# Kernel optimization log

Hardware: AMD Instinct MI355X
Metric: run time of the kernel (lower is better)

The kernel has to match this reference:

```python
import jax, jax.numpy as jnp
import numpy as np

LN_EPS = 1e-5  # torch LayerNorm default


def setup_inputs() -> dict:
    key = jax.random.key(0)
    ks = jax.random.split(key, 6)
    N, E, D = 50000, 800000, 128
    x = jax.random.normal(ks[0], (N, D), dtype=jnp.float32)
    edge_index = jax.random.randint(ks[1], (2, E), 0, N, dtype=jnp.int64)
    # Linear params (torch default-ish init scale)
    W = jax.random.normal(ks[2], (D, D), dtype=jnp.float32) / np.sqrt(D)
    b = jax.random.normal(ks[3], (D,), dtype=jnp.float32) * 0.01
    # LayerNorm params
    gamma = jnp.ones((D,), dtype=jnp.float32)
    beta = jnp.zeros((D,), dtype=jnp.float32)
    return {"x": x, "edge_index": edge_index, "W": W, "b": b,
            "gamma": gamma, "beta": beta}


def reference(x, edge_index, W, b, gamma, beta):
    N = x.shape[0]
    # add_self_loops
    loops = jnp.arange(N, dtype=edge_index.dtype)
    row = jnp.concatenate([edge_index[0], loops])  # sources (x_j)
    col = jnp.concatenate([edge_index[1], loops])  # targets (aggregate here)

    h = x @ W.T + b  # [N, D]

    # symmetric normalization: deg computed on row, includes self loops (deg>=1)
    deg = jax.ops.segment_sum(jnp.ones(row.shape, dtype=h.dtype), row,
                              num_segments=N)
    dis = deg ** -0.5
    norm = dis[row] * dis[col]  # [E+N]

    # gather-scale-scatter message passing (aggr='add')
    msg = norm[:, None] * h[row]              # [E+N, D]
    agg = jax.ops.segment_sum(msg, col, num_segments=N)  # [N, D]

    out = jax.nn.relu(agg)
    # dropout: identity (eval mode)
    mu = jnp.mean(out, axis=-1, keepdims=True)
    var = jnp.var(out, axis=-1, keepdims=True)
    out = (out - mu) * jax.lax.rsqrt(var + LN_EPS) * gamma + beta
    return out + x  # residual (in_channels == out_channels, no proj)
```

## Files before the change

### kernel.cpp

```cpp
#include <hip/hip_runtime.h>


#define D 128
#define CHSH 15
#define CHUNK (1 << CHSH)
#define NWORD 12500

typedef short bf16x8 __attribute__((ext_vector_type(8)));
typedef float f32x4 __attribute__((ext_vector_type(4)));

__device__ __forceinline__ unsigned short f2bf(float f) {
    unsigned u = __float_as_uint(f);
    return (unsigned short)((u + 0x7fffu + ((u >> 16) & 1u)) >> 16);
}
__device__ __forceinline__ float bf2f_lo(unsigned v) { return __uint_as_float(v << 16); }
__device__ __forceinline__ float bf2f_hi(unsigned v) { return __uint_as_float(v & 0xffff0000u); }

__global__ void __launch_bounds__(1024)
k_gemm_hist(const float* __restrict__ x, const float* __restrict__ W,
            const float* __restrict__ bias, unsigned short* __restrict__ hb,
            int nrows,
            const int* __restrict__ ei, int E, int n,
            unsigned char* __restrict__ degc, unsigned char* __restrict__ cntc,
            unsigned char* __restrict__ aux, int K) {
    __shared__ unsigned sm[NWORD];
    int bid = blockIdx.x;
    if (bid < 2 * K) {
        unsigned* hist = sm;
        bool is_cnt = bid < K;
        int c = is_cnt ? bid : bid - K;
        const int* vs = is_cnt ? (ei + E) : ei;
        for (int i = threadIdx.x; i < NWORD; i += 1024) hist[i] = 0u;
        __syncthreads();
        int e0 = c << CHSH;
        int e1 = e0 + CHUNK; if (e1 > E) e1 = E;
        if (is_cnt) {
            for (int e = e0 + threadIdx.x; e < e1; e += 1024) {
                int v = vs[e];
                unsigned sh = (v & 3) * 8;
                unsigned old = atomicAdd(&hist[v >> 2], 1u << sh);
                aux[e] = (unsigned char)(old >> sh);
            }
        } else {
            for (int e = e0 + threadIdx.x; e < e1; e += 1024) {
                int v = vs[e];
                atomicAdd(&hist[v >> 2], 1u << ((v & 3) * 8));
            }
        }
        __syncthreads();
        unsigned* dst = (unsigned*)((is_cnt ? cntc : degc) + (size_t)c * n);
        for (int i = threadIdx.x; i < NWORD; i += 1024) dst[i] = hist[i];
    } else {
        unsigned short* wf = (unsigned short*)sm;
        for (int s = threadIdx.x; s < D * D; s += 1024) {
            int j  = s & 7;
            int ln = (s >> 3) & 63;
            int g  = s >> 9;
            int kt = g & 3, nt = g >> 2;
            int rw = nt * 16 + (ln & 15);
            int cl = kt * 32 + (ln >> 4) * 8 + j;
            wf[s] = f2bf(W[rw * D + cl]);
        }
        __syncthreads();

        int wid = threadIdx.x >> 6, lane = threadIdx.x & 63;
        int m0 = (bid - 2 * K) * 256 + wid * 16;
        if (m0 >= nrows) return;
        int lo16 = lane & 15, quad = lane >> 4;
        const float* arow = x + (size_t)(m0 + lo16) * D + quad * 8;
        bf16x8 a[4];
        #pragma unroll
        for (int kt = 0; kt < 4; kt++) {
            float4 p = *(const float4*)(arow + kt * 32);
            float4 q = *(const float4*)(arow + kt * 32 + 4);
            bf16x8 av;
            av[0] = (short)f2bf(p.x); av[1] = (short)f2bf(p.y);
            av[2] = (short)f2bf(p.z); av[3] = (short)f2bf(p.w);
            av[4] = (short)f2bf(q.x); av[5] = (short)f2bf(q.y);
            av[6] = (short)f2bf(q.z); av[7] = (short)f2bf(q.w);
            a[kt] = av;
        }
        const bf16x8* wfv = (const bf16x8*)sm;
        #pragma unroll
        for (int nt = 0; nt < 8; nt++) {
            int n0 = nt * 16;
            float bj = bias[n0 + lo16];
            f32x4 acc = {bj, bj, bj, bj};
            #pragma unroll
            for (int kt = 0; kt < 4; kt++) {
                bf16x8 b = wfv[(nt * 4 + kt) * 64 + lane];
                acc = __builtin_amdgcn_mfma_f32_16x16x32_bf16(a[kt], b, acc, 0, 0, 0);
            }
            #pragma unroll
            for (int r = 0; r < 4; r++) {
                int gr = m0 + quad * 4 + r;
                hb[(size_t)gr * D + n0 + lo16] = f2bf(acc[r]);
            }
        }
    }
}

__global__ void k_partial(const unsigned char* __restrict__ degc,
                          const unsigned char* __restrict__ cntc,
                          float* __restrict__ dis, unsigned* __restrict__ cnt,
                          unsigned* __restrict__ partial, int n, int K) {
    __shared__ unsigned s[256];
    int t = threadIdx.x;
    int i = blockIdx.x * 256 + t;
    unsigned tot = 0;
    if (i < n) {
        unsigned d = 0;
        for (int c = 0; c < K; c++)
            d += __builtin_nontemporal_load(degc + (size_t)c * n + i);
        dis[i] = rsqrtf((float)d + 1.0f);
        for (int c = 0; c < K; c++) tot += cntc[(size_t)c * n + i];
        cnt[i] = tot;
    }
    s[t] = tot;
    __syncthreads();
    #pragma unroll
    for (int d = 128; d > 0; d >>= 1) {
        if (t < d) s[t] += s[t + d];
        __syncthreads();
    }
    if (t == 0) partial[blockIdx.x] = s[0];
}

__global__ void k_rowptrc(const unsigned* __restrict__ cnt, const unsigned char* __restrict__ cntc,
                          const unsigned* __restrict__ partial, int n, int E,
                          int* __restrict__ rowptr, unsigned char* __restrict__ pre8,
                          int K, int nb) {
    __shared__ unsigned ps[256];
    __shared__ unsigned base_sh;
    int t = threadIdx.x;
    unsigned pv = (t < nb) ? partial[t] : 0u;
    ps[t] = pv;
    __syncthreads();
    #pragma unroll
    for (int d = 1; d < 256; d <<= 1) {
        unsigned u = (t >= d) ? ps[t - d] : 0u;
        __syncthreads();
        ps[t] += u;
        __syncthreads();
    }
    if (t == blockIdx.x) base_sh = ps[t] - pv;
    __syncthreads();
    unsigned bbase = base_sh;
    int i = blockIdx.x * 256 + t;
    unsigned v = (i < n) ? cnt[i] : 0u;
    ps[t] = v;
    __syncthreads();
    #pragma unroll
    for (int d = 1; d < 256; d <<= 1) {
        unsigned u = (t >= d) ? ps[t - d] : 0u;
        __syncthreads();
        ps[t] += u;
        __syncthreads();
    }
    if (i < n) {
        int base = (int)(bbase + ps[t] - v);
        rowptr[i] = base;
        unsigned run = 0;
        for (int c = 0; c < K; c++) {
            pre8[(size_t)c * n + i] = (unsigned char)run;
            run += cntc[(size_t)c * n + i];
        }
    }
    if (blockIdx.x == 0 && t == 0) rowptr[n] = E;
}

__global__ void k_fill(const int* __restrict__ ei, int E, int n,
                       const int* __restrict__ rowptr, const unsigned char* __restrict__ pre8,
                       const unsigned char* __restrict__ aux,
                       unsigned short* __restrict__ srcs) {
    int e = blockIdx.x * 256 + threadIdx.x;
    if (e < E) {
        int r = __builtin_nontemporal_load(ei + e);
        int v = __builtin_nontemporal_load(ei + E + e);
        int c = e >> CHSH;
        int rank = __builtin_nontemporal_load(aux + e);
        int base = rowptr[v] + (int)pre8[(size_t)c * n + v];
        srcs[base + rank] = (unsigned short)r;
    }
}

__global__ void k_agg(const float* __restrict__ x, const unsigned short* __restrict__ hb,
                      const float* __restrict__ dis,
                      const int* __restrict__ rowptr, const unsigned short* __restrict__ srcs,
                      const float* __restrict__ gamma, const float* __restrict__ beta,
                      float* __restrict__ out, int n) {
    int wid = threadIdx.x >> 6, lane = threadIdx.x & 63;
    int row = blockIdx.x * 4 + wid;
    if (row >= n) return;
    int q = lane >> 4, t = lane & 15;
    float dc = dis[row];
    float acc[8];
    #pragma unroll
    for (int i = 0; i < 8; i++) acc[i] = 0.0f;
    if (q == 0) {
        uint4 u = ((const uint4*)(hb + (size_t)row * D))[t];
        float sn = dc * dc;
        acc[0] = sn * bf2f_lo(u.x); acc[1] = sn * bf2f_hi(u.x);
        acc[2] = sn * bf2f_lo(u.y); acc[3] = sn * bf2f_hi(u.y);
        acc[4] = sn * bf2f_lo(u.z); acc[5] = sn * bf2f_hi(u.z);
        acc[6] = sn * bf2f_lo(u.w); acc[7] = sn * bf2f_hi(u.w);
    }
    int s0 = rowptr[row];
    int len = rowptr[row + 1] - s0;
    for (int base = 0; base < len; base += 64) {
        int idx = base + lane;
        int sv = (idx < len) ? (int)__builtin_nontemporal_load(srcs + s0 + idx) : 0;
        float dv = (idx < len) ? dis[sv] : 0.0f;
        int m = len - base; if (m > 64) m = 64;
        int kmax = (m + 3) >> 2;
        int gcount = (kmax + 3) >> 2;
        for (int gg = 0; gg < gcount; gg++) {
            int jb = q + (gg << 4);
            int r0 = __shfl(sv, jb, 64);
            int r1 = __shfl(sv, jb + 4, 64);
            int r2 = __shfl(sv, jb + 8, 64);
            int r3 = __shfl(sv, jb + 12, 64);
            float w0 = dc * __shfl(dv, jb, 64);
            float w1 = dc * __shfl(dv, jb + 4, 64);
            float w2 = dc * __shfl(dv, jb + 8, 64);
            float w3 = dc * __shfl(dv, jb + 12, 64);
            uint4 u0 = ((const uint4*)(hb + ((size_t)r0 << 7)))[t];
            uint4 u1 = ((const uint4*)(hb + ((size_t)r1 << 7)))[t];
            uint4 u2 = ((const uint4*)(hb + ((size_t)r2 << 7)))[t];
            uint4 u3 = ((const uint4*)(hb + ((size_t)r3 << 7)))[t];
            acc[0] += w0 * bf2f_lo(u0.x); acc[1] += w0 * bf2f_hi(u0.x);
            acc[2] += w0 * bf2f_lo(u0.y); acc[3] += w0 * bf2f_hi(u0.y);
            acc[4] += w0 * bf2f_lo(u0.z); acc[5] += w0 * bf2f_hi(u0.z);
            acc[6] += w0 * bf2f_lo(u0.w); acc[7] += w0 * bf2f_hi(u0.w);
            acc[0] += w1 * bf2f_lo(u1.x); acc[1] += w1 * bf2f_hi(u1.x);
            acc[2] += w1 * bf2f_lo(u1.y); acc[3] += w1 * bf2f_hi(u1.y);
            acc[4] += w1 * bf2f_lo(u1.z); acc[5] += w1 * bf2f_hi(u1.z);
            acc[6] += w1 * bf2f_lo(u1.w); acc[7] += w1 * bf2f_hi(u1.w);
            acc[0] += w2 * bf2f_lo(u2.x); acc[1] += w2 * bf2f_hi(u2.x);
            acc[2] += w2 * bf2f_lo(u2.y); acc[3] += w2 * bf2f_hi(u2.y);
            acc[4] += w2 * bf2f_lo(u2.z); acc[5] += w2 * bf2f_hi(u2.z);
            acc[6] += w2 * bf2f_lo(u2.w); acc[7] += w2 * bf2f_hi(u2.w);
            acc[0] += w3 * bf2f_lo(u3.x); acc[1] += w3 * bf2f_hi(u3.x);
            acc[2] += w3 * bf2f_lo(u3.y); acc[3] += w3 * bf2f_hi(u3.y);
            acc[4] += w3 * bf2f_lo(u3.z); acc[5] += w3 * bf2f_hi(u3.z);
            acc[6] += w3 * bf2f_lo(u3.w); acc[7] += w3 * bf2f_hi(u3.w);
        }
    }
    #pragma unroll
    for (int i = 0; i < 8; i++) {
        acc[i] += __shfl_xor(acc[i], 16, 64);
        acc[i] += __shfl_xor(acc[i], 32, 64);
        acc[i] = acc[i] > 0.0f ? acc[i] : 0.0f;
    }
    float s1r = 0.0f, s2r = 0.0f;
    #pragma unroll
    for (int i = 0; i < 8; i++) { s1r += acc[i]; s2r += acc[i] * acc[i]; }
    #pragma unroll
    for (int mm = 8; mm >= 1; mm >>= 1) {
        s1r += __shfl_xor(s1r, mm, 64);
        s2r += __shfl_xor(s2r, mm, 64);
    }
    float mean = s1r * (1.0f / 128.0f);
    float var  = s2r * (1.0f / 128.0f) - mean * mean;
    float rstd = rsqrtf(var + 1e-5f);
    if (q == 0) {
        const f32x4* gr = (const f32x4*)gamma;
        const f32x4* br = (const f32x4*)beta;
        const f32x4* xr = (const f32x4*)(x + (size_t)row * D);
        f32x4* orow = (f32x4*)(out + (size_t)row * D);
        #pragma unroll
        for (int hf = 0; hf < 2; hf++) {
            f32x4 g = gr[2 * t + hf], b = br[2 * t + hf];
            f32x4 xx = __builtin_nontemporal_load(xr + 2 * t + hf);
            f32x4 o;
            o[0] = (acc[4 * hf + 0] - mean) * rstd * g[0] + b[0] + xx[0];
            o[1] = (acc[4 * hf + 1] - mean) * rstd * g[1] + b[1] + xx[1];
            o[2] = (acc[4 * hf + 2] - mean) * rstd * g[2] + b[2] + xx[2];
            o[3] = (acc[4 * hf + 3] - mean) * rstd * g[3] + b[3] + xx[3];
            __builtin_nontemporal_store(o, orow + 2 * t + hf);
        }
    }
}

extern "C" void kernel_launch(void* const* d_in, const int* in_sizes, int n_in,
                              void* d_out, int out_size, void* d_ws, size_t ws_size,
                              hipStream_t stream) {
    const float* x     = (const float*)d_in[0];
    const int*   ei    = (const int*)d_in[1];
    const float* W     = (const float*)d_in[2];
    const float* bias  = (const float*)d_in[3];
    const float* gamma = (const float*)d_in[4];
    const float* beta  = (const float*)d_in[5];
    int N = in_sizes[0] / D;
    int E = in_sizes[1] / 2;
    int nb  = (N + 255) / 256;
    int nbE = (E + 255) / 256;
    int K   = (E + CHUNK - 1) >> CHSH;
    int gemm_blocks = (N + 255) / 256;

    char* ws = (char*)d_ws;
    size_t off = 0;
    unsigned short* hb  = (unsigned short*)(ws + off); off += (size_t)N * D * 2;
    unsigned char* degc = (unsigned char*)(ws + off);  off += (size_t)K * N;
    unsigned char* cntc = (unsigned char*)(ws + off);  off += (size_t)K * N;
    float*    dis       = (float*)(ws + off);          off += (size_t)N * 4;
    unsigned* cnt       = (unsigned*)(ws + off);       off += (size_t)N * 4;
    int*      rowptr    = (int*)(ws + off);            off += (size_t)(N + 1) * 4;
    unsigned char* pre8 = (unsigned char*)(ws + off);  off += (size_t)K * N;
    unsigned* partial   = (unsigned*)(ws + off);       off += 256 * 4;
    unsigned char* aux  = (unsigned char*)(ws + off);  off += (size_t)E;
    off = (off + 1) & ~(size_t)1;
    unsigned short* srcs = (unsigned short*)(ws + off); off += (size_t)E * 2;
    float*    out       = (float*)d_out;

    k_gemm_hist<<<2 * K + gemm_blocks, 1024, 0, stream>>>(x, W, bias, hb, N,
                                                          ei, E, N, degc, cntc, aux, K);
    k_partial<<<nb, 256, 0, stream>>>(degc, cntc, dis, cnt, partial, N, K);
    k_rowptrc<<<nb, 256, 0, stream>>>(cnt, cntc, partial, N, E, rowptr, pre8, K, nb);
    k_fill<<<nbE, 256, 0, stream>>>(ei, E, N, rowptr, pre8, aux, srcs);
    k_agg<<<(N + 3) / 4, 256, 0, stream>>>(x, hb, dis, rowptr, srcs, gamma, beta, out, N);
}
```

Baseline: 177.0 us.

## Fuse post-GEMM stages into one cooperative kernel with grid syncs

Merges the degree/partial-sum, row-pointer scan, CSR fill and aggregation+LayerNorm kernels into a single persistent cooperative kernel that uses grid.sync between phases. The goal is to remove three kernel launch boundaries and their launch/drain overhead. In exchange, the grid is limited to the number of co-resident blocks, so the aggregation phase loops over rows with fewer blocks, and each grid barrier has its own cost. If the cooperative launch fails, it falls back to the old separate kernels.

```diff
diff --git a/kernel.cpp b/kernel.cpp
--- a/kernel.cpp
+++ b/kernel.cpp
@@ -1,4 +1,7 @@
 #include <hip/hip_runtime.h>
+#include <hip/hip_cooperative_groups.h>
+
+namespace cg = cooperative_groups;
 
 
 #define D 128
@@ -95,6 +98,189 @@
             for (int r = 0; r < 4; r++) {
                 int gr = m0 + quad * 4 + r;
                 hb[(size_t)gr * D + n0 + lo16] = f2bf(acc[r]);
+            }
+        }
+    }
+}
+
+__global__ void __launch_bounds__(256, 8)
+k_coop(const float* __restrict__ x, const unsigned short* __restrict__ hb,
+       const unsigned char* __restrict__ degc, const unsigned char* __restrict__ cntc,
+       const unsigned char* __restrict__ aux, const int* __restrict__ ei,
+       float* __restrict__ dis, unsigned* __restrict__ cnt,
+       int* __restrict__ rowptr, unsigned char* __restrict__ pre8,
+       unsigned* __restrict__ partial, unsigned short* __restrict__ srcs,
+       const float* __restrict__ gamma, const float* __restrict__ beta,
+       float* __restrict__ out, int n, int E, int K, int nb) {
+    cg::grid_group grid = cg::this_grid();
+    int bid = blockIdx.x, t = threadIdx.x;
+    int NB = gridDim.x;
+    __shared__ unsigned ps[256];
+    __shared__ unsigned base_sh;
+
+    for (int b = bid; b < nb; b += NB) {
+        int i = b * 256 + t;
+        unsigned tot = 0;
+        if (i < n) {
+            unsigned d = 0;
+            for (int c = 0; c < K; c++)
+                d += __builtin_nontemporal_load(degc + (size_t)c * n + i);
+            dis[i] = rsqrtf((float)d + 1.0f);
+            for (int c = 0; c < K; c++) tot += cntc[(size_t)c * n + i];
+            cnt[i] = tot;
+        }
+        ps[t] = tot;
+        __syncthreads();
+        #pragma unroll
+        for (int d = 128; d > 0; d >>= 1) {
+            if (t < d) ps[t] += ps[t + d];
+            __syncthreads();
+        }
+        if (t == 0) partial[b] = ps[0];
+        __syncthreads();
+    }
+    grid.sync();
+
+    for (int b = bid; b < nb; b += NB) {
+        unsigned pv = (t < nb) ? partial[t] : 0u;
+        ps[t] = pv;
+        __syncthreads();
+        #pragma unroll
+        for (int d = 1; d < 256; d <<= 1) {
+            unsigned u = (t >= d) ? ps[t - d] : 0u;
+            __syncthreads();
+            ps[t] += u;
+            __syncthreads();
+        }
+        if (t == b) base_sh = ps[t] - pv;
+        __syncthreads();
+        unsigned bbase = base_sh;
+        int i = b * 256 + t;
+        unsigned v = (i < n) ? cnt[i] : 0u;
+        ps[t] = v;
+        __syncthreads();
+        #pragma unroll
+        for (int d = 1; d < 256; d <<= 1) {
+            unsigned u = (t >= d) ? ps[t - d] : 0u;
+            __syncthreads();
+            ps[t] += u;
+            __syncthreads();
+        }
+        if (i < n) {
+            int base = (int)(bbase + ps[t] - v);
+            rowptr[i] = base;
+            unsigned run = 0;
+            for (int c = 0; c < K; c++) {
+                pre8[(size_t)c * n + i] = (unsigned char)run;
+                run += cntc[(size_t)c * n + i];
+            }
+        }
+        if (b == 0 && t == 0) rowptr[n] = E;
+        __syncthreads();
+    }
+    grid.sync();
+
+    for (int e = bid * 256 + t; e < E; e += NB * 256) {
+        int r = __builtin_nontemporal_load(ei + e);
+        int v = __builtin_nontemporal_load(ei + E + e);
+        int c = e >> CHSH;
+        int rank = __builtin_nontemporal_load(aux + e);
+        int base = rowptr[v] + (int)pre8[(size_t)c * n + v];
+        srcs[base + rank] = (unsigned short)r;
+    }
+    grid.sync();
+
+    int wid = t >> 6, lane = t & 63;
+    int q = lane >> 4, tt = lane & 15;
+    int nrg = (n + 3) >> 2;
+    for (int rg = bid; rg < nrg; rg += NB) {
+        int row = rg * 4 + wid;
+        if (row >= n) continue;
+        float dc = dis[row];
+        float acc[8];
+        #pragma unroll
+        for (int i = 0; i < 8; i++) acc[i] = 0.0f;
+        if (q == 0) {
+            uint4 u = ((const uint4*)(hb + (size_t)row * D))[tt];
+            float sn = dc * dc;
+            acc[0] = sn * bf2f_lo(u.x); acc[1] = sn * bf2f_hi(u.x);
+            acc[2] = sn * bf2f_lo(u.y); acc[3] = sn * bf2f_hi(u.y);
+            acc[4] = sn * bf2f_lo(u.z); acc[5] = sn * bf2f_hi(u.z);
+            acc[6] = sn * bf2f_lo(u.w); acc[7] = sn * bf2f_hi(u.w);
+        }
+        int s0 = rowptr[row];
+        int len = rowptr[row + 1] - s0;
+        for (int base = 0; base < len; base += 64) {
+            int idx = base + lane;
+            int sv = (idx < len) ? (int)__builtin_nontemporal_load(srcs + s0 + idx) : 0;
+            float dv = (idx < len) ? dis[sv] : 0.0f;
+            int m = len - base; if (m > 64) m = 64;
+            int kmax = (m + 3) >> 2;
+            int gcount = (kmax + 3) >> 2;
+            for (int gg = 0; gg < gcount; gg++) {
+                int jb = q + (gg << 4);
+                int r0 = __shfl(sv, jb, 64);
+                int r1 = __shfl(sv, jb + 4, 64);
+                int r2 = __shfl(sv, jb + 8, 64);
+                int r3 = __shfl(sv, jb + 12, 64);
+                float w0 = dc * __shfl(dv, jb, 64);
+                float w1 = dc * __shfl(dv, jb + 4, 64);
+                float w2 = dc * __shfl(dv, jb + 8, 64);
+                float w3 = dc * __shfl(dv, jb + 12, 64);
+                uint4 u0 = ((const uint4*)(hb + ((size_t)r0 << 7)))[tt];
+                uint4 u1 = ((const uint4*)(hb + ((size_t)r1 << 7)))[tt];
+                uint4 u2 = ((const uint4*)(hb + ((size_t)r2 << 7)))[tt];
+                uint4 u3 = ((const uint4*)(hb + ((size_t)r3 << 7)))[tt];
+                acc[0] += w0 * bf2f_lo(u0.x); acc[1] += w0 * bf2f_hi(u0.x);
+                acc[2] += w0 * bf2f_lo(u0.y); acc[3] += w0 * bf2f_hi(u0.y);
+                acc[4] += w0 * bf2f_lo(u0.z); acc[5] += w0 * bf2f_hi(u0.z);
+                acc[6] += w0 * bf2f_lo(u0.w); acc[7] += w0 * bf2f_hi(u0.w);
+                acc[0] += w1 * bf2f_lo(u1.x); acc[1] += w1 * bf2f_hi(u1.x);
+                acc[2] += w1 * bf2f_lo(u1.y); acc[3] += w1 * bf2f_hi(u1.y);
+                acc[4] += w1 * bf2f_lo(u1.z); acc[5] += w1 * bf2f_hi(u1.z);
+                acc[6] += w1 * bf2f_lo(u1.w); acc[7] += w1 * bf2f_hi(u1.w);
+                acc[0] += w2 * bf2f_lo(u2.x); acc[1] += w2 * bf2f_hi(u2.x);
+                acc[2] += w2 * bf2f_lo(u2.y); acc[3] += w2 * bf2f_hi(u2.y);
+                acc[4] += w2 * bf2f_lo(u2.z); acc[5] += w2 * bf2f_hi(u2.z);
+                acc[6] += w2 * bf2f_lo(u2.w); acc[7] += w2 * bf2f_hi(u2.w);
+                acc[0] += w3 * bf2f_lo(u3.x); acc[1] += w3 * bf2f_hi(u3.x);
+                acc[2] += w3 * bf2f_lo(u3.y); acc[3] += w3 * bf2f_hi(u3.y);
+                acc[4] += w3 * bf2f_lo(u3.z); acc[5] += w3 * bf2f_hi(u3.z);
+                acc[6] += w3 * bf2f_lo(u3.w); acc[7] += w3 * bf2f_hi(u3.w);
+            }
+        }
+        #pragma unroll
+        for (int i = 0; i < 8; i++) {
+            acc[i] += __shfl_xor(acc[i], 16, 64);
+            acc[i] += __shfl_xor(acc[i], 32, 64);
+            acc[i] = acc[i] > 0.0f ? acc[i] : 0.0f;
+        }
+        float s1r = 0.0f, s2r = 0.0f;
+        #pragma unroll
+        for (int i = 0; i < 8; i++) { s1r += acc[i]; s2r += acc[i] * acc[i]; }
+        #pragma unroll
+        for (int mm = 8; mm >= 1; mm >>= 1) {
+            s1r += __shfl_xor(s1r, mm, 64);
+            s2r += __shfl_xor(s2r, mm, 64);
+        }
+        float mean = s1r * (1.0f / 128.0f);
+        float var  = s2r * (1.0f / 128.0f) - mean * mean;
+        float rstd = rsqrtf(var + 1e-5f);
+        if (q == 0) {
+            const f32x4* gr = (const f32x4*)gamma;
+            const f32x4* br = (const f32x4*)beta;
+            const f32x4* xr = (const f32x4*)(x + (size_t)row * D);
+            f32x4* orow = (f32x4*)(out + (size_t)row * D);
+            #pragma unroll
+            for (int hf = 0; hf < 2; hf++) {
+                f32x4 g = gr[2 * tt + hf], b = br[2 * tt + hf];
+                f32x4 xx = __builtin_nontemporal_load(xr + 2 * tt + hf);
+                f32x4 o;
+                o[0] = (acc[4 * hf + 0] - mean) * rstd * g[0] + b[0] + xx[0];
+                o[1] = (acc[4 * hf + 1] - mean) * rstd * g[1] + b[1] + xx[1];
+                o[2] = (acc[4 * hf + 2] - mean) * rstd * g[2] + b[2] + xx[2];
+                o[3] = (acc[4 * hf + 3] - mean) * rstd * g[3] + b[3] + xx[3];
+                __builtin_nontemporal_store(o, orow + 2 * tt + hf);
             }
         }
     }
@@ -313,10 +499,37 @@
     unsigned short* srcs = (unsigned short*)(ws + off); off += (size_t)E * 2;
     float*    out       = (float*)d_out;
 
+    static int NB_cached = 0;
+    if (NB_cached == 0) {
+        int bpc = 0;
+        if (hipOccupancyMaxActiveBlocksPerMultiprocessor(&bpc, k_coop, 256, 0) != hipSuccess || bpc < 1)
+            bpc = 2;
+        int dev = 0;
+        hipGetDevice(&dev);
+        hipDeviceProp_t prop;
+        int ncu = 256;
+        if (hipGetDeviceProperties(&prop, dev) == hipSuccess && prop.multiProcessorCount > 0)
+            ncu = prop.multiProcessorCount;
+        long long nbl = (long long)bpc * ncu;
+        if (nbl > 2048) nbl = 2048;
+        if (nbl < 64) nbl = 64;
+        NB_cached = (int)nbl;
+    }
+    int NB = NB_cached;
+
     k_gemm_hist<<<2 * K + gemm_blocks, 1024, 0, stream>>>(x, W, bias, hb, N,
                                                           ei, E, N, degc, cntc, aux, K);
-    k_partial<<<nb, 256, 0, stream>>>(degc, cntc, dis, cnt, partial, N, K);
-    k_rowptrc<<<nb, 256, 0, stream>>>(cnt, cntc, partial, N, E, rowptr, pre8, K, nb);
-    k_fill<<<nbE, 256, 0, stream>>>(ei, E, N, rowptr, pre8, aux, srcs);
-    k_agg<<<(N + 3) / 4, 256, 0, stream>>>(x, hb, dis, rowptr, srcs, gamma, beta, out, N);
-}
+
+    void* args[] = { (void*)&x, (void*)&hb, (void*)&degc, (void*)&cntc, (void*)&aux,
+                     (void*)&ei, (void*)&dis, (void*)&cnt, (void*)&rowptr, (void*)&pre8,
+                     (void*)&partial, (void*)&srcs, (void*)&gamma, (void*)&beta,
+                     (void*)&out, (void*)&N, (void*)&E, (void*)&K, (void*)&nb };
+    hipError_t cerr = hipLaunchCooperativeKernel((const void*)k_coop, dim3(NB), dim3(256),
+                                                 args, 0, stream);
+    if (cerr != hipSuccess) {
+        k_partial<<<nb, 256, 0, stream>>>(degc, cntc, dis, cnt, partial, N, K);
+        k_rowptrc<<<nb, 256, 0, stream>>>(cnt, cntc, partial, N, E, rowptr, pre8, K, nb);
+        k_fill<<<nbE, 256, 0, stream>>>(ei, E, N, rowptr, pre8, aux, srcs);
+        k_agg<<<(N + 3) / 4, 256, 0, stream>>>(x, hb, dis, rowptr, srcs, gamma, beta, out, N);
+    }
+}
```

After: 532.1 us. 3.01x slower.

## Merge partial-sum and rowptr kernels into single-pass decoupled-lookback scan

Applied to the files above, without the earlier changes.

Replaces the two-kernel scan (block partial sums, then a block-level rescan plus per-node scan) with one kernel. Each block publishes its aggregate with a ready flag and spin-waits on the flags of all predecessor blocks to get its base offset. The partial array is zeroed inside the histogram kernel, so one launch and one pass over the per-chunk count arrays go away. In exchange it relies on blocks being scheduled in order to avoid deadlock, and later blocks repeatedly poll global atomics.

```diff
diff --git a/kernel.cpp b/kernel.cpp
--- a/kernel.cpp
+++ b/kernel.cpp
@@ -22,10 +22,11 @@
             int nrows,
             const int* __restrict__ ei, int E, int n,
             unsigned char* __restrict__ degc, unsigned char* __restrict__ cntc,
-            unsigned char* __restrict__ aux, int K) {
+            unsigned char* __restrict__ aux, unsigned* __restrict__ partial, int K) {
     __shared__ unsigned sm[NWORD];
     int bid = blockIdx.x;
     if (bid < 2 * K) {
+        if (bid == 0 && threadIdx.x < 256) partial[threadIdx.x] = 0u;
         unsigned* hist = sm;
         bool is_cnt = bid < K;
         int c = is_cnt ? bid : bid - K;
@@ -100,73 +101,58 @@
     }
 }
 
-__global__ void k_partial(const unsigned char* __restrict__ degc,
-                          const unsigned char* __restrict__ cntc,
-                          float* __restrict__ dis, unsigned* __restrict__ cnt,
-                          unsigned* __restrict__ partial, int n, int K) {
-    __shared__ unsigned s[256];
-    int t = threadIdx.x;
-    int i = blockIdx.x * 256 + t;
+__global__ void k_scan(const unsigned char* __restrict__ degc,
+                       const unsigned char* __restrict__ cntc,
+                       float* __restrict__ dis, int* __restrict__ rowptr,
+                       unsigned char* __restrict__ pre8,
+                       unsigned* __restrict__ partial, int n, int E, int K) {
+    __shared__ unsigned ps[256];
+    __shared__ unsigned bb_sh;
+    int t = threadIdx.x, bid = blockIdx.x;
+    int i = bid * 256 + t;
     unsigned tot = 0;
     if (i < n) {
         unsigned d = 0;
         for (int c = 0; c < K; c++)
             d += __builtin_nontemporal_load(degc + (size_t)c * n + i);
         dis[i] = rsqrtf((float)d + 1.0f);
-        for (int c = 0; c < K; c++) tot += cntc[(size_t)c * n + i];
-        cnt[i] = tot;
-    }
-    s[t] = tot;
-    __syncthreads();
-    #pragma unroll
-    for (int d = 128; d > 0; d >>= 1) {
-        if (t < d) s[t] += s[t + d];
-        __syncthreads();
-    }
-    if (t == 0) partial[blockIdx.x] = s[0];
-}
-
-__global__ void k_rowptrc(const unsigned* __restrict__ cnt, const unsigned char* __restrict__ cntc,
-                          const unsigned* __restrict__ partial, int n, int E,
-                          int* __restrict__ rowptr, unsigned char* __restrict__ pre8,
-                          int K, int nb) {
-    __shared__ unsigned ps[256];
-    __shared__ unsigned base_sh;
-    int t = threadIdx.x;
-    unsigned pv = (t < nb) ? partial[t] : 0u;
-    ps[t] = pv;
-    __syncthreads();
-    #pragma unroll
-    for (int d = 1; d < 256; d <<= 1) {
-        unsigned u = (t >= d) ? ps[t - d] : 0u;
-        __syncthreads();
-        ps[t] += u;
-        __syncthreads();
-    }
-    if (t == blockIdx.x) base_sh = ps[t] - pv;
-    __syncthreads();
-    unsigned bbase = base_sh;
-    int i = blockIdx.x * 256 + t;
-    unsigned v = (i < n) ? cnt[i] : 0u;
-    ps[t] = v;
-    __syncthreads();
-    #pragma unroll
-    for (int d = 1; d < 256; d <<= 1) {
-        unsigned u = (t >= d) ? ps[t - d] : 0u;
-        __syncthreads();
-        ps[t] += u;
-        __syncthreads();
-    }
-    if (i < n) {
-        int base = (int)(bbase + ps[t] - v);
-        rowptr[i] = base;
         unsigned run = 0;
         for (int c = 0; c < K; c++) {
             pre8[(size_t)c * n + i] = (unsigned char)run;
             run += cntc[(size_t)c * n + i];
         }
-    }
-    if (blockIdx.x == 0 && t == 0) rowptr[n] = E;
+        tot = run;
+    }
+    ps[t] = tot;
+    __syncthreads();
+    #pragma unroll
+    for (int d = 1; d < 256; d <<= 1) {
+        unsigned u = (t >= d) ? ps[t - d] : 0u;
+        __syncthreads();
+        ps[t] += u;
+        __syncthreads();
+    }
+    unsigned incl = ps[t];
+    unsigned agg  = ps[255];
+    if (t < 64) {
+        if (t == 0) atomicExch(&partial[bid], agg | 0x80000000u);
+        unsigned sum = 0;
+        for (int j0 = 0; j0 < bid; j0 += 64) {
+            int j = j0 + t;
+            if (j < bid) {
+                unsigned v;
+                do { v = atomicAdd(&partial[j], 0u); } while (!(v & 0x80000000u));
+                sum += v & 0x7fffffffu;
+            }
+        }
+        #pragma unroll
+        for (int mm = 32; mm >= 1; mm >>= 1) sum += __shfl_xor(sum, mm, 64);
+        if (t == 0) bb_sh = sum;
+    }
+    __syncthreads();
+    unsigned bbase = bb_sh;
+    if (i < n) rowptr[i] = (int)(bbase + incl - tot);
+    if (bid == 0 && t == 0) rowptr[n] = E;
 }
 
 __global__ void k_fill(const int* __restrict__ ei, int E, int n,
@@ -304,7 +290,6 @@
     unsigned char* degc = (unsigned char*)(ws + off);  off += (size_t)K * N;
     unsigned char* cntc = (unsigned char*)(ws + off);  off += (size_t)K * N;
     float*    dis       = (float*)(ws + off);          off += (size_t)N * 4;
-    unsigned* cnt       = (unsigned*)(ws + off);       off += (size_t)N * 4;
     int*      rowptr    = (int*)(ws + off);            off += (size_t)(N + 1) * 4;
     unsigned char* pre8 = (unsigned char*)(ws + off);  off += (size_t)K * N;
     unsigned* partial   = (unsigned*)(ws + off);       off += 256 * 4;
@@ -314,9 +299,9 @@
     float*    out       = (float*)d_out;
 
     k_gemm_hist<<<2 * K + gemm_blocks, 1024, 0, stream>>>(x, W, bias, hb, N,
-                                                          ei, E, N, degc, cntc, aux, K);
-    k_partial<<<nb, 256, 0, stream>>>(degc, cntc, dis, cnt, partial, N, K);
-    k_rowptrc<<<nb, 256, 0, stream>>>(cnt, cntc, partial, N, E, rowptr, pre8, K, nb);
+                                                          ei, E, N, degc, cntc, aux,
+                                                          partial, K);
+    k_scan<<<nb, 256, 0, stream>>>(degc, cntc, dis, rowptr, pre8, partial, N, E, K);
     k_fill<<<nbE, 256, 0, stream>>>(ei, E, N, rowptr, pre8, aux, srcs);
     k_agg<<<(N + 3) / 4, 256, 0, stream>>>(x, hb, dis, rowptr, srcs, gamma, beta, out, N);
 }
```

After: 174.1 us (median of 2 runs). Within noise of the previous version (-1.6%).
